# Kernel tuning notes

Measured on AMD Instinct MI355X. Metric: run time of the kernel, lower is better.

The kernel has to match this reference:

```python
import jax, jax.numpy as jnp
import numpy as np
from jax import lax

T, B, NIN, H, NOUT = 256, 64, 256, 2048, 256
DT, TAU, SIGMA = 20.0, 100.0, 0.05
DECAY = DT / TAU                      # alpha in the leaky-Euler update
NOISE_SCALE = SIGMA * float(np.sqrt(2.0 / DECAY))
MAX_INIT_STEPS = 100
ATOL = 0.1


def setup_inputs() -> dict:
    key = jax.random.key(0)
    k1, k2, k3, k4 = jax.random.split(key, 4)
    x = jax.random.normal(k1, (T, B, NIN), dtype=jnp.float32)
    W_ih = jax.random.normal(k2, (H, NIN), dtype=jnp.float32) / np.sqrt(NIN)
    # w_rec_init='diag': strong diagonal plus small random recurrent weights
    W_hh = 0.5 * jnp.eye(H, dtype=jnp.float32) + 0.1 * jax.random.normal(k3, (H, H), dtype=jnp.float32) / np.sqrt(H)
    b = jnp.zeros((H,), dtype=jnp.float32)
    W_out = jax.random.normal(k4, (NOUT, H), dtype=jnp.float32) / np.sqrt(H)
    return {"x": x, "W_ih": W_ih, "W_hh": W_hh, "b": b, "W_out": W_out}


def reference(x, W_ih, W_hh, b, W_out):
    base = jax.random.key(42)

    def cell(h, x_t, k):
        # leaky RNN step: h' = (1-a)h + a*relu(W_ih x + W_hh h + b + noise)
        pre = x_t @ W_ih.T + h @ W_hh.T + b
        pre = pre + NOISE_SCALE * jax.random.normal(k, pre.shape, dtype=pre.dtype)
        return (1.0 - DECAY) * h + DECAY * jax.nn.relu(pre)

    # ---- init_hidden_: up to 100 probe iterations of 2 steps on x[:2, 0:1] ----
    x_probe = x[:2, :1]                       # [2, 1, NIN], broadcasts vs h [B, H]
    h0_init = jnp.zeros((B, H), dtype=x.dtype)

    def init_body(carry, i):
        h0, stable, done = carry
        k = jax.random.fold_in(base, i)
        ka, kb = jax.random.split(k)
        h1 = cell(h0, x_probe[0], ka)
        h2 = cell(h1, x_probe[1], kb)
        close = jnp.max(jnp.abs(h2 - h0)) <= ATOL
        stable_new = jnp.where(done, stable, jnp.where(close, stable + 1, 0))
        trigger = (~done) & close & (stable_new >= 4)   # return pre-update h0
        done_new = done | trigger
        h0_new = jnp.where(done_new, h0, h2)
        return (h0_new, stable_new, done_new), None

    (h0, _, _), _ = lax.scan(init_body, (h0_init, jnp.int32(0), jnp.bool_(False)),
                             jnp.arange(MAX_INIT_STEPS))

    # ---- main unroll over T steps ----
    ks = jax.random.split(jax.random.fold_in(base, 1_000_000), T)

    def step(h, inp):
        x_t, k = inp
        h_new = cell(h, x_t, k)
        return h_new, h_new

    _, hidden = lax.scan(step, h0, (x, ks))   # [T, B, H]
    output = hidden @ W_out.T                 # [T, B, NOUT]
    return output, hidden
```

## Files before the change

kernel.cpp:

```cpp
#include <hip/hip_runtime.h>

typedef unsigned int u32;
typedef unsigned short u16;
typedef __bf16 bf16x8 __attribute__((ext_vector_type(8)));
typedef u16 us8 __attribute__((ext_vector_type(8)));
typedef u32 u32x4 __attribute__((ext_vector_type(4)));
typedef float f32x4 __attribute__((ext_vector_type(4)));

#define T_N 256
#define B_N 64
#define NIN_N 256
#define H_N 2048
#define NOUT_N 256
#define BH (B_N * H_N)
#define OUT_SZ (T_N * B_N * NOUT_N)

#define LDS_WHH_H 0
#define LDS_WHH_L 65536
#define LDS_RBUF  131072
#define LDS_RED   139264
#define LDS_BYTES 139328

struct U2 { u32 x, y; };

__device__ __forceinline__ u32 rotl32(u32 v, int r) { return (v << r) | (v >> (32 - r)); }

__device__ __forceinline__ U2 tf2x32(U2 k, U2 x) {
  u32 ks0 = k.x, ks1 = k.y, ks2 = k.x ^ k.y ^ 0x1BD11BDAu;
  x.x += ks0; x.y += ks1;
#define TFR(a) x.x += x.y; x.y = rotl32(x.y,(a)); x.y ^= x.x;
  TFR(13) TFR(15) TFR(26) TFR(6)
  x.x += ks1; x.y += ks2 + 1u;
  TFR(17) TFR(29) TFR(16) TFR(24)
  x.x += ks2; x.y += ks0 + 2u;
  TFR(13) TFR(15) TFR(26) TFR(6)
  x.x += ks0; x.y += ks1 + 3u;
  TFR(17) TFR(29) TFR(16) TFR(24)
  x.x += ks1; x.y += ks2 + 4u;
  TFR(13) TFR(15) TFR(26) TFR(6)
  x.x += ks2; x.y += ks0 + 5u;
#undef TFR
  return x;
}

__device__ __forceinline__ float jax_normal(u32 bits) {
  float f = __uint_as_float((bits >> 9) | 0x3f800000u) - 1.0f;
  const float lo = -0.99999994f;
  float u = fmaf(f, 2.0f, lo);
  u = fmaxf(u, lo);
  float w = -log1pf(-u * u);
  float p;
  if (w < 5.0f) {
    w = w - 2.5f;
    p =            2.81022636e-08f;
    p = fmaf(p, w, 3.43273939e-07f);
    p = fmaf(p, w, -3.5233877e-06f);
    p = fmaf(p, w, -4.39150654e-06f);
    p = fmaf(p, w, 0.00021858087f);
    p = fmaf(p, w, -0.00125372503f);
    p = fmaf(p, w, -0.00417768164f);
    p = fmaf(p, w, 0.246640727f);
    p = fmaf(p, w, 1.50140941f);
  } else {
    w = sqrtf(w) - 3.0f;
    p =            -0.000200214257f;
    p = fmaf(p, w, 0.000100950558f);
    p = fmaf(p, w, 0.00134934322f);
    p = fmaf(p, w, -0.00367342844f);
    p = fmaf(p, w, 0.00573950773f);
    p = fmaf(p, w, -0.0076224613f);
    p = fmaf(p, w, 0.00943887047f);
    p = fmaf(p, w, 1.00167406f);
    p = fmaf(p, w, 2.83297682f);
  }
  return 1.41421354f * (p * u);
}

__device__ __forceinline__ u16 f2bf(float f) {
  u32 x = __float_as_uint(f);
  u32 r = (x + 0x7FFFu + ((x >> 16) & 1u)) >> 16;
  return (u16)r;
}
__device__ __forceinline__ float bf2f(u16 b) { return __uint_as_float(((u32)b) << 16); }

__device__ __forceinline__ bf16x8 ld8(const u16* p) {
  us8 v = *reinterpret_cast<const us8*>(p);
  return __builtin_bit_cast(bf16x8, v);
}
__device__ __forceinline__ f32x4 mfma16(bf16x8 a, bf16x8 b, f32x4 c) {
  return __builtin_amdgcn_mfma_f32_16x16x32_bf16(a, b, c, 0, 0, 0);
}

__device__ __forceinline__ void st_agent_u16(u16* p, u16 v) {
  __hip_atomic_store(p, v, __ATOMIC_RELAXED, __HIP_MEMORY_SCOPE_AGENT);
}
__device__ __forceinline__ void st_agent_u32(u32* p, u32 v, int order) {
  if (order) __hip_atomic_store(p, v, __ATOMIC_RELEASE, __HIP_MEMORY_SCOPE_AGENT);
  else       __hip_atomic_store(p, v, __ATOMIC_RELAXED, __HIP_MEMORY_SCOPE_AGENT);
}
__device__ __forceinline__ u32 ld_agent_u32(const u32* p) {
  return __hip_atomic_load(p, __ATOMIC_RELAXED, __HIP_MEMORY_SCOPE_AGENT);
}

#define GLD16(AP, V) \
  asm volatile( \
    "global_load_dwordx4 %0, %16, off offset:-4096 sc0 sc1\n\t" \
    "global_load_dwordx4 %1, %16, off sc0 sc1\n\t" \
    "global_load_dwordx4 %2, %17, off offset:-4096 sc0 sc1\n\t" \
    "global_load_dwordx4 %3, %17, off sc0 sc1\n\t" \
    "global_load_dwordx4 %4, %18, off offset:-4096 sc0 sc1\n\t" \
    "global_load_dwordx4 %5, %18, off sc0 sc1\n\t" \
    "global_load_dwordx4 %6, %19, off offset:-4096 sc0 sc1\n\t" \
    "global_load_dwordx4 %7, %19, off sc0 sc1\n\t" \
    "global_load_dwordx4 %8, %20, off offset:-4096 sc0 sc1\n\t" \
    "global_load_dwordx4 %9, %20, off sc0 sc1\n\t" \
    "global_load_dwordx4 %10, %21, off offset:-4096 sc0 sc1\n\t" \
    "global_load_dwordx4 %11, %21, off sc0 sc1\n\t" \
    "global_load_dwordx4 %12, %22, off offset:-4096 sc0 sc1\n\t" \
    "global_load_dwordx4 %13, %22, off sc0 sc1\n\t" \
    "global_load_dwordx4 %14, %23, off offset:-4096 sc0 sc1\n\t" \
    "global_load_dwordx4 %15, %23, off sc0 sc1\n\t" \
    "s_waitcnt vmcnt(0)" \
    : "=&v"(V##0), "=&v"(V##1), "=&v"(V##2), "=&v"(V##3), \
      "=&v"(V##4), "=&v"(V##5), "=&v"(V##6), "=&v"(V##7), \
      "=&v"(V##8), "=&v"(V##9), "=&v"(V##10), "=&v"(V##11), \
      "=&v"(V##12), "=&v"(V##13), "=&v"(V##14), "=&v"(V##15) \
    : "v"(AP + 2048), "v"(AP + 3 * 2048), "v"(AP + 5 * 2048), "v"(AP + 7 * 2048), \
      "v"(AP + 9 * 2048), "v"(AP + 11 * 2048), "v"(AP + 13 * 2048), "v"(AP + 15 * 2048) \
    : "memory")

__global__ void __launch_bounds__(256) pack_b_kernel(const float* __restrict__ W,
    u16* __restrict__ hi, u16* __restrict__ lo, int K, int Cshift) {
  int tid = blockIdx.x * 256 + threadIdx.x;
  int lane = tid & 63;
  size_t tile = tid >> 6;
  int C = 1 << Cshift;
  int jt = (int)(tile >> Cshift), c = (int)(tile & (C - 1));
  int row = jt * 16 + (lane & 15);
  int k0 = c * 32 + (lane >> 4) * 8;
  const float* src = W + (size_t)row * K + k0;
  us8 vh, vl;
#pragma unroll
  for (int j = 0; j < 8; ++j) {
    float w = src[j];
    u16 hb = f2bf(w);
    vh[j] = hb;
    vl[j] = f2bf(w - bf2f(hb));
  }
  *reinterpret_cast<us8*>(hi + tile * 512 + lane * 8) = vh;
  *reinterpret_cast<us8*>(lo + tile * 512 + lane * 8) = vl;
}

__global__ void __launch_bounds__(256) pack_x_kernel(const float* __restrict__ x,
    u16* __restrict__ hi, u16* __restrict__ lo) {
  int tid = blockIdx.x * 256 + threadIdx.x;
  int t = tid >> 11;
  int r = tid & 2047;
  int lane = r & 63, piece = r >> 6;
  int c = piece >> 2, g = piece & 3;
  int row = g * 16 + (lane & 15);
  int k0 = c * 32 + (lane >> 4) * 8;
  const float* src = x + (size_t)t * (B_N * NIN_N) + (size_t)row * NIN_N + k0;
  us8 vh, vl;
#pragma unroll
  for (int j = 0; j < 8; ++j) {
    float w = src[j];
    u16 hb = f2bf(w);
    vh[j] = hb;
    vl[j] = f2bf(w - bf2f(hb));
  }
  size_t off = (size_t)t * 16384 + (size_t)piece * 512 + lane * 8;
  *reinterpret_cast<us8*>(hi + off) = vh;
  *reinterpret_cast<us8*>(lo + off) = vl;
}

__global__ void __launch_bounds__(256) probe_proj(const float* __restrict__ x,
    const float* __restrict__ Wih, const float* __restrict__ bias, float* __restrict__ xpj) {
  int g = blockIdx.x * 256 + threadIdx.x;
  int p = g >> 11, col = g & 2047;
  const float* xr = x + (size_t)p * (B_N * NIN_N);
  const float* wr = Wih + (size_t)col * NIN_N;
  float s = 0.f;
#pragma unroll 4
  for (int k = 0; k < NIN_N; ++k) s = fmaf(xr[k], wr[k], s);
  xpj[p * H_N + col] = s + bias[col];
}

__global__ void __launch_bounds__(256) xproj_gemm(const u16* __restrict__ xp_hi,
    const u16* __restrict__ xp_lo, const u16* __restrict__ wih_hi,
    const u16* __restrict__ wih_lo, const float* __restrict__ bias,
    float* __restrict__ xout) {
  int lane = threadIdx.x & 63, wvq = threadIdx.x >> 6;
  int t = blockIdx.x >> 7, jt16 = blockIdx.x & 127;
  const u16* ah = xp_hi + (size_t)t * 16384 + wvq * 512 + lane * 8;
  const u16* al = xp_lo + (size_t)t * 16384 + wvq * 512 + lane * 8;
  const u16* bh = wih_hi + (size_t)jt16 * 4096 + lane * 8;
  const u16* bl = wih_lo + (size_t)jt16 * 4096 + lane * 8;
  f32x4 z = {0.f, 0.f, 0.f, 0.f};
  f32x4 a0 = z, a1 = z, a2 = z;
#pragma unroll
  for (int c = 0; c < 8; ++c) {
    bf16x8 xh = ld8(ah + c * 2048), xl = ld8(al + c * 2048);
    bf16x8 wh = ld8(bh + c * 512),  wl = ld8(bl + c * 512);
    a0 = mfma16(xh, wh, a0);
    a1 = mfma16(xh, wl, a1);
    a2 = mfma16(xl, wh, a2);
  }
  f32x4 acc = (a0 + a1) + a2;
  int col = jt16 * 16 + (lane & 15);
  int q = lane >> 4;
  float bc = bias[col];
#pragma unroll
  for (int r = 0; r < 4; ++r) {
    int row = wvq * 16 + q * 4 + r;
    xout[(size_t)t * BH + (size_t)row * H_N + col] = acc[r] + bc;
  }
}

__global__ void setup_keys(U2* ka, U2* kb, U2* ks) {
  int i = threadIdx.x;
  U2 base{0u, 42u};
  if (i < 104) {
    U2 ki = tf2x32(base, U2{0u, (u32)i});
    ka[i] = tf2x32(ki, U2{0u, 0u});
    kb[i] = tf2x32(ki, U2{0u, 1u});
  }
  U2 km = tf2x32(base, U2{0u, 1000000u});
  ks[i] = tf2x32(km, U2{0u, (u32)i});
}

__global__ void __launch_bounds__(256) zero_bufs(u32* hx0w, u32* hx0lw, u32* bar) {
  int g = blockIdx.x * 256 + threadIdx.x;
  if (g < BH / 2) { hx0w[g] = 0u; hx0lw[g] = 0u; }
  if (g < 1024) bar[g] = 0u;
}

struct RnnParams {
  const u16 *whh_hi, *whh_lo;
  const float* xpj;
  float* hidden;
  u16 *hx0, *hx1, *hx2;
  u16 *hx0l, *hx1l, *hx2l;
  u16 *hxS0, *hxS1, *hxS2;
  const U2 *ka, *kb, *ks;
  u32 *slots, *mslot;
  u32 *initflag, *scanflag;
};

__global__ void __launch_bounds__(512) rnn_persistent(RnnParams P) {
  extern __shared__ char smem[];
  u16* lwhh_h = (u16*)(smem + LDS_WHH_H);
  u16* lwhh_l = (u16*)(smem + LDS_WHH_L);
  f32x4* rbuf = (f32x4*)(smem + LDS_RBUF);
  float* red  = (float*)(smem + LDS_RED);

  const int lane = threadIdx.x & 63;
  const int wv = threadIdx.x >> 6;
  const int rg = wv >> 2;
  const int kh = wv & 3;
  const int blk = blockIdx.x;
  const int jt16 = blk & 127;
  const int rh = blk >> 7;
  const int bqg = rh * 2 + rg;
  const int q = lane >> 4;
  const int row = bqg * 16 + q * 4 + kh;
  const int col = jt16 * 16 + (lane & 15);
  const u32 idx = (u32)row * H_N + (u32)col;
  const u32 xoff = ((u32)((col >> 5) * 4 + (row >> 4)) * 64
                    + (u32)(((col >> 3) & 3) * 16 + (row & 15))) * 8 + (u32)(col & 7);

  {
    const us8* sh = (const us8*)(P.whh_hi + (size_t)jt16 * 32768);
    const us8* sl = (const us8*)(P.whh_lo + (size_t)jt16 * 32768);
    us8* dh = (us8*)lwhh_h;
    us8* dl = (us8*)lwhh_l;
#pragma unroll 2
    for (int i = threadIdx.x; i < 4096; i += 512) { dh[i] = sh[i]; dl[i] = sl[i]; }
    __syncthreads();
  }
  const u16* bhp = lwhh_h + kh * 8192 + lane * 8;
  const u16* blp = lwhh_l + kh * 8192 + lane * 8;

  const u32* fl_init = P.initflag + rh * 128 + kh * 32;
  const u32* fl_scan = P.scanflag + rh * 128 + kh * 32;

  auto poll32 = [&](const u32* fl, u32 need) {
    const u32* p = fl + (lane & 31);
    for (;;) {
      u32 v;
      asm volatile("global_load_dword %0, %1, off sc0 sc1\n\ts_waitcnt vmcnt(0)"
                   : "=v"(v) : "v"(p) : "memory");
      if (__all(v >= need)) break;
      __builtin_amdgcn_s_sleep(1);
    }
  };

  auto publish = [&](u32* flagarr, u32 val) {
    asm volatile("s_waitcnt vmcnt(0)" ::: "memory");
    __syncthreads();
    if (threadIdx.x == 0) st_agent_u32(flagarr + blk, val, 1);
  };

  u32 ebar = 0;
  auto bar_agg = [&]() {
    ++ebar;
    asm volatile("s_waitcnt vmcnt(0)" ::: "memory");
    __syncthreads();
    if (wv == 0) {
      if (lane == 0) {
        float m = red[0];
#pragma unroll
        for (int w2 = 1; w2 < 8; ++w2) m = fmaxf(m, red[w2]);
        st_agent_u32(P.mslot + blk, __float_as_uint(m), 0);
        st_agent_u32(P.slots + blk, ebar, 1);
      }
      const u32* ps = P.slots + lane * 4;
      for (;;) {
        u32x4 pr;
        asm volatile("global_load_dwordx4 %0, %1, off sc0 sc1\n\ts_waitcnt vmcnt(0)"
                     : "=&v"(pr) : "v"(ps) : "memory");
        u32 mn = pr.x < pr.y ? pr.x : pr.y;
        u32 mn2 = pr.z < pr.w ? pr.z : pr.w;
        mn = mn < mn2 ? mn : mn2;
        if (__all(mn >= ebar)) break;
        __builtin_amdgcn_s_sleep(1);
      }
      float m = fmaxf(fmaxf(__uint_as_float(ld_agent_u32(P.mslot + lane * 4 + 0)),
                            __uint_as_float(ld_agent_u32(P.mslot + lane * 4 + 1))),
                      fmaxf(__uint_as_float(ld_agent_u32(P.mslot + lane * 4 + 2)),
                            __uint_as_float(ld_agent_u32(P.mslot + lane * 4 + 3))));
#pragma unroll
      for (int o = 32; o >= 1; o >>= 1) m = fmaxf(m, __shfl_down(m, o));
      if (lane == 0) ((u32*)red)[8] = (m <= 0.1f) ? 1u : 0u;
    }
    __syncthreads();
  };

  auto reduce_av = [&](f32x4 acc) -> float {
    rbuf[wv * 64 + lane] = acc;
    __syncthreads();
    const float* rb = (const float*)(rbuf + rg * 256);
    return rb[lane * 4 + kh] + rb[256 + lane * 4 + kh]
         + rb[512 + lane * 4 + kh] + rb[768 + lane * 4 + kh];
  };

  auto gemm_hi = [&](const u16* hx_in) -> float {
    const u16* ap = hx_in + bqg * 512 + kh * 32768 + lane * 8;
    u32x4 A0, A1, A2, A3, A4, A5, A6, A7, A8, A9, A10, A11, A12, A13, A14, A15;
    GLD16(ap, A);
    f32x4 z = {0.f, 0.f, 0.f, 0.f};
    f32x4 a0 = z, a1 = z, a2 = z, a3 = z;
#define HSTEP(c, AV) { bf16x8 bh_ = ld8(bhp + (c) * 512); bf16x8 bl_ = ld8(blp + (c) * 512); \
    bf16x8 ah_ = __builtin_bit_cast(bf16x8, AV); \
    if ((c) & 1) { a2 = mfma16(ah_, bh_, a2); a3 = mfma16(ah_, bl_, a3); } \
    else { a0 = mfma16(ah_, bh_, a0); a1 = mfma16(ah_, bl_, a1); } }
    HSTEP(0, A0)  HSTEP(1, A1)  HSTEP(2, A2)  HSTEP(3, A3)
    HSTEP(4, A4)  HSTEP(5, A5)  HSTEP(6, A6)  HSTEP(7, A7)
    HSTEP(8, A8)  HSTEP(9, A9)  HSTEP(10, A10) HSTEP(11, A11)
    HSTEP(12, A12) HSTEP(13, A13) HSTEP(14, A14) HSTEP(15, A15)
#undef HSTEP
    return reduce_av((a0 + a1) + (a2 + a3));
  };

  auto gemm_hilo = [&](const u16* hx_in, const u16* hx_lo) -> float {
    const u16* aph = hx_in + bqg * 512 + kh * 32768 + lane * 8;
    const u16* apl = hx_lo + bqg * 512 + kh * 32768 + lane * 8;
    f32x4 z = {0.f, 0.f, 0.f, 0.f};
    f32x4 a0 = z, a1 = z, a2 = z, a3 = z, a4 = z, a5 = z;
    {
      u32x4 H0, H1, H2, H3, H4, H5, H6, H7, H8, H9, H10, H11, H12, H13, H14, H15;
      GLD16(aph, H);
#define ISTEP(c, AV) { bf16x8 bh_ = ld8(bhp + (c) * 512); bf16x8 bl_ = ld8(blp + (c) * 512); \
      bf16x8 ah_ = __builtin_bit_cast(bf16x8, AV); \
      if ((c) & 1) { a3 = mfma16(ah_, bh_, a3); a4 = mfma16(ah_, bl_, a4); } \
      else { a0 = mfma16(ah_, bh_, a0); a1 = mfma16(ah_, bl_, a1); } }
      ISTEP(0, H0)  ISTEP(1, H1)  ISTEP(2, H2)  ISTEP(3, H3)
      ISTEP(4, H4)  ISTEP(5, H5)  ISTEP(6, H6)  ISTEP(7, H7)
      ISTEP(8, H8)  ISTEP(9, H9)  ISTEP(10, H10) ISTEP(11, H11)
      ISTEP(12, H12) ISTEP(13, H13) ISTEP(14, H14) ISTEP(15, H15)
#undef ISTEP
    }
    {
      u32x4 L0, L1, L2, L3, L4, L5, L6, L7, L8, L9, L10, L11, L12, L13, L14, L15;
      GLD16(apl, L);
#define LSTEP(c, AV) { bf16x8 bh_ = ld8(bhp + (c) * 512); \
      bf16x8 al_ = __builtin_bit_cast(bf16x8, AV); \
      if ((c) & 1) { a5 = mfma16(al_, bh_, a5); } \
      else { a2 = mfma16(al_, bh_, a2); } }
      LSTEP(0, L0)  LSTEP(1, L1)  LSTEP(2, L2)  LSTEP(3, L3)
      LSTEP(4, L4)  LSTEP(5, L5)  LSTEP(6, L6)  LSTEP(7, L7)
      LSTEP(8, L8)  LSTEP(9, L9)  LSTEP(10, L10) LSTEP(11, L11)
      LSTEP(12, L12) LSTEP(13, L13) LSTEP(14, L14) LSTEP(15, L15)
#undef LSTEP
    }
    return reduce_av(((a0 + a1) + (a2 + a3)) + (a4 + a5));
  };

  auto make_noise = [&](U2 key) -> float {
    U2 o = tf2x32(key, U2{0u, idx});
    return jax_normal(o.x ^ o.y);
  };

  const float NS = 0.15811388300841897f;
  const float xv0 = P.xpj[col];
  const float xv1 = P.xpj[H_N + col];

  u16* hxs[3]  = {P.hx0, P.hx1, P.hx2};
  u16* hxls[3] = {P.hx0l, P.hx1l, P.hx2l};
  int i0 = 0, i1 = 1, i2 = 2;
  float hp0 = 0.f;
  int stable = 0;
  float nzA = make_noise(P.ka[0]);
  float nzB = 0.f;

#pragma unroll 1
  for (int it = 0; it < 100; ++it) {
    float av = gemm_hilo(hxs[i0], hxls[i0]);
    float pre = av + xv0 + NS * nzA;
    float hp1 = 0.8f * hp0 + 0.2f * fmaxf(pre, 0.f);
    { u16 hb = f2bf(hp1);
      st_agent_u16(hxs[i1] + xoff, hb);
      st_agent_u16(hxls[i1] + xoff, f2bf(hp1 - bf2f(hb))); }
    publish(P.initflag, (u32)(it + 1));
    nzB = make_noise(P.kb[it]);
    poll32(fl_init, (u32)(it + 1));

    av = gemm_hilo(hxs[i1], hxls[i1]);
    pre = av + xv1 + NS * nzB;
    float hp2 = 0.8f * hp1 + 0.2f * fmaxf(pre, 0.f);
    { u16 hb = f2bf(hp2);
      st_agent_u16(hxs[i2] + xoff, hb);
      st_agent_u16(hxls[i2] + xoff, f2bf(hp2 - bf2f(hb))); }
    float lmax = fabsf(hp2 - hp0);
#pragma unroll
    for (int off = 32; off >= 1; off >>= 1)
      lmax = fmaxf(lmax, __shfl_down(lmax, off));
    if (lane == 0) red[wv] = lmax;
    nzA = make_noise(P.ka[it + 1]);
    bar_agg();

    bool close = (((u32*)red)[8] & 1u) != 0u;
    if (close) {
      if (++stable >= 4) break;
    } else stable = 0;
    int tmp = i0; i0 = i2; i2 = tmp;
    hp0 = hp2;
  }

  u16* bufs[3] = {P.hxS0, P.hxS1, P.hxS2};
  st_agent_u16(bufs[0] + xoff, f2bf(hp0));
  publish(P.scanflag, 1u);
  float nzS = make_noise(P.ks[0]);
  float xv = P.hidden[idx];
  float hp = hp0;
#pragma unroll 1
  for (int t = 0; t < T_N; ++t) {
    poll32(fl_scan, (u32)(t + 1));
    float av = gemm_hi(bufs[t % 3]);
    float pre = av + xv + NS * nzS;
    float hn = 0.8f * hp + 0.2f * fmaxf(pre, 0.f);
    hp = hn;
    P.hidden[(size_t)t * BH + idx] = hn;
    if (t != T_N - 1) {
      st_agent_u16(bufs[(t + 1) % 3] + xoff, f2bf(hn));
      publish(P.scanflag, (u32)(t + 2));
      nzS = make_noise(P.ks[t + 1]);
      xv = P.hidden[(size_t)(t + 1) * BH + idx];
    }
  }
}

__global__ void __launch_bounds__(256) out_gemm(const float* __restrict__ hidden,
    const u16* __restrict__ wo_hi, const u16* __restrict__ wo_lo, float* __restrict__ out) {
  int lane = threadIdx.x & 63, wv = threadIdx.x >> 6;
  int mb = blockIdx.x * 64 + wv * 16;
  int arow = mb + (lane & 15);
  int q = lane >> 4;
  f32x4 acc[16];
#pragma unroll
  for (int n = 0; n < 16; ++n) acc[n] = {0.f, 0.f, 0.f, 0.f};
  const float* ap = hidden + (size_t)arow * H_N + q * 8;
#pragma unroll 2
  for (int c = 0; c < 64; ++c) {
    const float4* a4 = reinterpret_cast<const float4*>(ap + c * 32);
    float4 f0 = a4[0], f1 = a4[1];
    us8 av;
    av[0] = f2bf(f0.x); av[1] = f2bf(f0.y); av[2] = f2bf(f0.z); av[3] = f2bf(f0.w);
    av[4] = f2bf(f1.x); av[5] = f2bf(f1.y); av[6] = f2bf(f1.z); av[7] = f2bf(f1.w);
    bf16x8 a = __builtin_bit_cast(bf16x8, av);
#pragma unroll
    for (int n = 0; n < 16; ++n) {
      bf16x8 bh = ld8(wo_hi + ((size_t)(n * 64 + c) * 64 + lane) * 8);
      bf16x8 bl = ld8(wo_lo + ((size_t)(n * 64 + c) * 64 + lane) * 8);
      acc[n] = mfma16(a, bh, acc[n]);
      acc[n] = mfma16(a, bl, acc[n]);
    }
  }
#pragma unroll
  for (int n = 0; n < 16; ++n)
#pragma unroll
    for (int r = 0; r < 4; ++r)
      out[(size_t)(mb + q * 4 + r) * NOUT_N + n * 16 + (lane & 15)] = acc[n][r];
}

extern "C" void kernel_launch(void* const* d_in, const int* in_sizes, int n_in,
                              void* d_out, int out_size, void* d_ws, size_t ws_size,
                              hipStream_t stream) {
  const float* x = (const float*)d_in[0];
  const float* W_ih = (const float*)d_in[1];
  const float* W_hh = (const float*)d_in[2];
  const float* bias = (const float*)d_in[3];
  const float* W_out = (const float*)d_in[4];
  float* out = (float*)d_out;

  char* ws = (char*)d_ws;
  size_t off = 0;
  auto alloc = [&](size_t bytes) -> void* {
    void* p = ws + off;
    off += (bytes + 255) & ~(size_t)255;
    return p;
  };
  u16* whh_hi = (u16*)alloc(8388608);
  u16* whh_lo = (u16*)alloc(8388608);
  u16* wih_hi = (u16*)alloc(1048576);
  u16* wih_lo = (u16*)alloc(1048576);
  u16* wout_hi = (u16*)alloc(1048576);
  u16* wout_lo = (u16*)alloc(1048576);
  u16* xp_hi = (u16*)alloc(8388608);
  u16* xp_lo = (u16*)alloc(8388608);
  float* xpj = (float*)alloc(16384);
  u16* hx0 = (u16*)alloc(262144);
  u16* hx1 = (u16*)alloc(262144);
  u16* hx2 = (u16*)alloc(262144);
  u16* hx0l = (u16*)alloc(262144);
  u16* hx1l = (u16*)alloc(262144);
  u16* hx2l = (u16*)alloc(262144);
  u16* hxS0 = (u16*)alloc(262144);
  u16* hxS1 = (u16*)alloc(262144);
  u16* hxS2 = (u16*)alloc(262144);
  U2* ka = (U2*)alloc(832);
  U2* kb = (U2*)alloc(832);
  U2* ks = (U2*)alloc(2048);
  u32* bar = (u32*)alloc(4096);

  float* hidden = out + OUT_SZ;

  hipLaunchKernelGGL(pack_b_kernel, dim3(2048), dim3(256), 0, stream, W_hh, whh_hi, whh_lo, 2048, 6);
  hipLaunchKernelGGL(pack_b_kernel, dim3(256), dim3(256), 0, stream, W_ih, wih_hi, wih_lo, 256, 3);
  hipLaunchKernelGGL(pack_b_kernel, dim3(256), dim3(256), 0, stream, W_out, wout_hi, wout_lo, 2048, 6);
  hipLaunchKernelGGL(pack_x_kernel, dim3(2048), dim3(256), 0, stream, x, xp_hi, xp_lo);
  hipLaunchKernelGGL(probe_proj, dim3(16), dim3(256), 0, stream, x, W_ih, bias, xpj);
  hipLaunchKernelGGL(setup_keys, dim3(1), dim3(256), 0, stream, ka, kb, ks);
  hipLaunchKernelGGL(zero_bufs, dim3(256), dim3(256), 0, stream, (u32*)hx0, (u32*)hx0l, bar);
  hipLaunchKernelGGL(xproj_gemm, dim3(32768), dim3(256), 0, stream, xp_hi, xp_lo, wih_hi, wih_lo, bias, hidden);

  RnnParams P;
  P.whh_hi = whh_hi; P.whh_lo = whh_lo;
  P.xpj = xpj;
  P.hidden = hidden;
  P.hx0 = hx0; P.hx1 = hx1; P.hx2 = hx2;
  P.hx0l = hx0l; P.hx1l = hx1l; P.hx2l = hx2l;
  P.hxS0 = hxS0; P.hxS1 = hxS1; P.hxS2 = hxS2;
  P.ka = ka; P.kb = kb; P.ks = ks;
  P.slots = bar; P.mslot = bar + 256;
  P.initflag = bar + 512; P.scanflag = bar + 768;

  static bool attr_set = false;
  if (!attr_set) {
    hipFuncSetAttribute((const void*)rnn_persistent,
                        hipFuncAttributeMaxDynamicSharedMemorySize, LDS_BYTES);
    attr_set = true;
  }

  void* kargs[] = {(void*)&P};
  hipLaunchCooperativeKernel((const void*)rnn_persistent, dim3(256), dim3(512), kargs, LDS_BYTES, stream);

  hipLaunchKernelGGL(out_gemm, dim3(256), dim3(256), 0, stream, hidden, wout_hi, wout_lo, out);
}
```

Baseline: 4.955 ms.

## Repartition persistent RNN blocks by batch group with full-K split and narrower flag polling

Each block now owns a 16-row batch group and 32 hidden columns, with its eight waves splitting the full K dimension. Previously blocks split batch into halves and covered 16 columns with a four-way K split. The W_hh hi part is kept in LDS while the lo correction is read from global memory. Each block now waits on only 8 producer flags per wave instead of 32, cutting dependency fan-in and poll traffic, and the hidden-state store is moved after publishing the next step's flag. The cost is an 8-way LDS reduction and global loads of the lo weights on every step, which may add latency.

```diff
diff --git a/kernel.cpp b/kernel.cpp
--- a/kernel.cpp
+++ b/kernel.cpp
@@ -15,11 +15,10 @@
 #define BH (B_N * H_N)
 #define OUT_SZ (T_N * B_N * NOUT_N)
 
-#define LDS_WHH_H 0
-#define LDS_WHH_L 65536
-#define LDS_RBUF  131072
-#define LDS_RED   139264
-#define LDS_BYTES 139328
+#define LDS_W    0
+#define LDS_RBUF 131072
+#define LDS_RED  147456
+#define LDS_BYTES 147520
 
 struct U2 { u32 x, y; };
 
@@ -102,7 +101,23 @@
   return __hip_atomic_load(p, __ATOMIC_RELAXED, __HIP_MEMORY_SCOPE_AGENT);
 }
 
-#define GLD16(AP, V) \
+#define GLD8(AP, V) \
+  asm volatile( \
+    "global_load_dwordx4 %0, %8, off offset:-4096 sc0 sc1\n\t" \
+    "global_load_dwordx4 %1, %8, off sc0 sc1\n\t" \
+    "global_load_dwordx4 %2, %9, off offset:-4096 sc0 sc1\n\t" \
+    "global_load_dwordx4 %3, %9, off sc0 sc1\n\t" \
+    "global_load_dwordx4 %4, %10, off offset:-4096 sc0 sc1\n\t" \
+    "global_load_dwordx4 %5, %10, off sc0 sc1\n\t" \
+    "global_load_dwordx4 %6, %11, off offset:-4096 sc0 sc1\n\t" \
+    "global_load_dwordx4 %7, %11, off sc0 sc1\n\t" \
+    "s_waitcnt vmcnt(0)" \
+    : "=&v"(V##0), "=&v"(V##1), "=&v"(V##2), "=&v"(V##3), \
+      "=&v"(V##4), "=&v"(V##5), "=&v"(V##6), "=&v"(V##7) \
+    : "v"(AP + 2048), "v"(AP + 3 * 2048), "v"(AP + 5 * 2048), "v"(AP + 7 * 2048) \
+    : "memory")
+
+#define GLD8HL(APH, APL, V, W) \
   asm volatile( \
     "global_load_dwordx4 %0, %16, off offset:-4096 sc0 sc1\n\t" \
     "global_load_dwordx4 %1, %16, off sc0 sc1\n\t" \
@@ -123,10 +138,10 @@
     "s_waitcnt vmcnt(0)" \
     : "=&v"(V##0), "=&v"(V##1), "=&v"(V##2), "=&v"(V##3), \
       "=&v"(V##4), "=&v"(V##5), "=&v"(V##6), "=&v"(V##7), \
-      "=&v"(V##8), "=&v"(V##9), "=&v"(V##10), "=&v"(V##11), \
-      "=&v"(V##12), "=&v"(V##13), "=&v"(V##14), "=&v"(V##15) \
-    : "v"(AP + 2048), "v"(AP + 3 * 2048), "v"(AP + 5 * 2048), "v"(AP + 7 * 2048), \
-      "v"(AP + 9 * 2048), "v"(AP + 11 * 2048), "v"(AP + 13 * 2048), "v"(AP + 15 * 2048) \
+      "=&v"(W##0), "=&v"(W##1), "=&v"(W##2), "=&v"(W##3), \
+      "=&v"(W##4), "=&v"(W##5), "=&v"(W##6), "=&v"(W##7) \
+    : "v"(APH + 2048), "v"(APH + 3 * 2048), "v"(APH + 5 * 2048), "v"(APH + 7 * 2048), \
+      "v"(APL + 2048), "v"(APL + 3 * 2048), "v"(APL + 5 * 2048), "v"(APL + 7 * 2048) \
     : "memory")
 
 __global__ void __launch_bounds__(256) pack_b_kernel(const float* __restrict__ W,
@@ -249,43 +264,45 @@
 
 __global__ void __launch_bounds__(512) rnn_persistent(RnnParams P) {
   extern __shared__ char smem[];
-  u16* lwhh_h = (u16*)(smem + LDS_WHH_H);
-  u16* lwhh_l = (u16*)(smem + LDS_WHH_L);
+  u16* lW = (u16*)(smem + LDS_W);
   f32x4* rbuf = (f32x4*)(smem + LDS_RBUF);
   float* red  = (float*)(smem + LDS_RED);
 
-  const int lane = threadIdx.x & 63;
-  const int wv = threadIdx.x >> 6;
-  const int rg = wv >> 2;
-  const int kh = wv & 3;
+  const int tid = threadIdx.x;
+  const int lane = tid & 63;
+  const int wv = tid >> 6;
+  const int ke = wv;
+  const int cs_own = wv >> 2;
+  const int r_own = wv & 3;
   const int blk = blockIdx.x;
-  const int jt16 = blk & 127;
-  const int rh = blk >> 7;
-  const int bqg = rh * 2 + rg;
-  const int q = lane >> 4;
-  const int row = bqg * 16 + q * 4 + kh;
-  const int col = jt16 * 16 + (lane & 15);
+  const int bg = blk >> 6;
+  const int ct = blk & 63;
+  const int row = bg * 16 + (lane >> 4) * 4 + r_own;
+  const int col = ct * 32 + cs_own * 16 + (lane & 15);
   const u32 idx = (u32)row * H_N + (u32)col;
   const u32 xoff = ((u32)((col >> 5) * 4 + (row >> 4)) * 64
                     + (u32)(((col >> 3) & 3) * 16 + (row & 15))) * 8 + (u32)(col & 7);
 
   {
-    const us8* sh = (const us8*)(P.whh_hi + (size_t)jt16 * 32768);
-    const us8* sl = (const us8*)(P.whh_lo + (size_t)jt16 * 32768);
-    us8* dh = (us8*)lwhh_h;
-    us8* dl = (us8*)lwhh_l;
-#pragma unroll 2
-    for (int i = threadIdx.x; i < 4096; i += 512) { dh[i] = sh[i]; dl[i] = sl[i]; }
+    const us8* src = (const us8*)P.whh_hi;
+    us8* dst = (us8*)lW;
+#pragma unroll 4
+    for (int i = tid; i < 8192; i += 512) {
+      int cs_ = i >> 12, rem = i & 4095;
+      dst[i] = src[(size_t)(ct * 2 + cs_) * 4096 + rem];
+    }
     __syncthreads();
   }
-  const u16* bhp = lwhh_h + kh * 8192 + lane * 8;
-  const u16* blp = lwhh_l + kh * 8192 + lane * 8;
-
-  const u32* fl_init = P.initflag + rh * 128 + kh * 32;
-  const u32* fl_scan = P.scanflag + rh * 128 + kh * 32;
-
-  auto poll32 = [&](const u32* fl, u32 need) {
-    const u32* p = fl + (lane & 31);
+  const u16* lwb0 = lW + ke * 4096 + lane * 8;
+  const u16* lwb1 = lW + 32768 + ke * 4096 + lane * 8;
+  const u16* wlo0 = P.whh_lo + (size_t)(ct * 2 + 0) * 32768 + ke * 4096 + lane * 8;
+  const u16* wlo1 = P.whh_lo + (size_t)(ct * 2 + 1) * 32768 + ke * 4096 + lane * 8;
+
+  const u32* ifw = P.initflag + bg * 64 + ke * 8;
+  const u32* sfw = P.scanflag + bg * 64 + ke * 8;
+
+  auto pollW = [&](const u32* fw, u32 need) {
+    const u32* p = fw + (lane & 7);
     for (;;) {
       u32 v;
       asm volatile("global_load_dword %0, %1, off sc0 sc1\n\ts_waitcnt vmcnt(0)"
@@ -298,7 +315,7 @@
   auto publish = [&](u32* flagarr, u32 val) {
     asm volatile("s_waitcnt vmcnt(0)" ::: "memory");
     __syncthreads();
-    if (threadIdx.x == 0) st_agent_u32(flagarr + blk, val, 1);
+    if (tid == 0) st_agent_u32(flagarr + blk, val, 1);
   };
 
   u32 ebar = 0;
@@ -336,64 +353,75 @@
     __syncthreads();
   };
 
-  auto reduce_av = [&](f32x4 acc) -> float {
-    rbuf[wv * 64 + lane] = acc;
+  auto reduce_sum = [&](f32x4 o0, f32x4 o1) -> float {
+    rbuf[(wv * 2 + 0) * 64 + lane] = o0;
+    rbuf[(wv * 2 + 1) * 64 + lane] = o1;
     __syncthreads();
-    const float* rb = (const float*)(rbuf + rg * 256);
-    return rb[lane * 4 + kh] + rb[256 + lane * 4 + kh]
-         + rb[512 + lane * 4 + kh] + rb[768 + lane * 4 + kh];
-  };
-
-  auto gemm_hi = [&](const u16* hx_in) -> float {
-    const u16* ap = hx_in + bqg * 512 + kh * 32768 + lane * 8;
-    u32x4 A0, A1, A2, A3, A4, A5, A6, A7, A8, A9, A10, A11, A12, A13, A14, A15;
-    GLD16(ap, A);
+    const float* rb = (const float*)rbuf;
+    int o = cs_own * 256 + lane * 4 + r_own;
+    float av = rb[o];
+    av += rb[o + 512];  av += rb[o + 1024]; av += rb[o + 1536];
+    av += rb[o + 2048]; av += rb[o + 2560]; av += rb[o + 3072]; av += rb[o + 3584];
+    return av;
+  };
+
+  auto gemm_sc = [&](const u16* hx_in, f32x4& o0, f32x4& o1) {
+    const u16* ap = hx_in + bg * 512 + ke * 16384 + lane * 8;
+    u32x4 A0, A1, A2, A3, A4, A5, A6, A7;
+    GLD8(ap, A);
     f32x4 z = {0.f, 0.f, 0.f, 0.f};
-    f32x4 a0 = z, a1 = z, a2 = z, a3 = z;
-#define HSTEP(c, AV) { bf16x8 bh_ = ld8(bhp + (c) * 512); bf16x8 bl_ = ld8(blp + (c) * 512); \
-    bf16x8 ah_ = __builtin_bit_cast(bf16x8, AV); \
-    if ((c) & 1) { a2 = mfma16(ah_, bh_, a2); a3 = mfma16(ah_, bl_, a3); } \
-    else { a0 = mfma16(ah_, bh_, a0); a1 = mfma16(ah_, bl_, a1); } }
-    HSTEP(0, A0)  HSTEP(1, A1)  HSTEP(2, A2)  HSTEP(3, A3)
-    HSTEP(4, A4)  HSTEP(5, A5)  HSTEP(6, A6)  HSTEP(7, A7)
-    HSTEP(8, A8)  HSTEP(9, A9)  HSTEP(10, A10) HSTEP(11, A11)
-    HSTEP(12, A12) HSTEP(13, A13) HSTEP(14, A14) HSTEP(15, A15)
-#undef HSTEP
-    return reduce_av((a0 + a1) + (a2 + a3));
-  };
-
-  auto gemm_hilo = [&](const u16* hx_in, const u16* hx_lo) -> float {
-    const u16* aph = hx_in + bqg * 512 + kh * 32768 + lane * 8;
-    const u16* apl = hx_lo + bqg * 512 + kh * 32768 + lane * 8;
+    {
+      f32x4 a0 = z, a1 = z, a2 = z, a3 = z;
+#define SSTEP(j, AV) { bf16x8 bh_ = ld8(lwb0 + (j) * 512); bf16x8 bl_ = ld8(wlo0 + (j) * 512); \
+      bf16x8 ah_ = __builtin_bit_cast(bf16x8, AV); \
+      if ((j) & 1) { a2 = mfma16(ah_, bh_, a2); a3 = mfma16(ah_, bl_, a3); } \
+      else { a0 = mfma16(ah_, bh_, a0); a1 = mfma16(ah_, bl_, a1); } }
+      SSTEP(0, A0) SSTEP(1, A1) SSTEP(2, A2) SSTEP(3, A3)
+      SSTEP(4, A4) SSTEP(5, A5) SSTEP(6, A6) SSTEP(7, A7)
+#undef SSTEP
+      o0 = (a0 + a1) + (a2 + a3);
+    }
+    {
+      f32x4 a0 = z, a1 = z, a2 = z, a3 = z;
+#define SSTEP(j, AV) { bf16x8 bh_ = ld8(lwb1 + (j) * 512); bf16x8 bl_ = ld8(wlo1 + (j) * 512); \
+      bf16x8 ah_ = __builtin_bit_cast(bf16x8, AV); \
+      if ((j) & 1) { a2 = mfma16(ah_, bh_, a2); a3 = mfma16(ah_, bl_, a3); } \
+      else { a0 = mfma16(ah_, bh_, a0); a1 = mfma16(ah_, bl_, a1); } }
+      SSTEP(0, A0) SSTEP(1, A1) SSTEP(2, A2) SSTEP(3, A3)
+      SSTEP(4, A4) SSTEP(5, A5) SSTEP(6, A6) SSTEP(7, A7)
+#undef SSTEP
+      o1 = (a0 + a1) + (a2 + a3);
+    }
+  };
+
+  auto gemm_in = [&](const u16* hxh, const u16* hxl, f32x4& o0, f32x4& o1) {
+    const u16* aph = hxh + bg * 512 + ke * 16384 + lane * 8;
+    const u16* apl = hxl + bg * 512 + ke * 16384 + lane * 8;
+    u32x4 H0, H1, H2, H3, H4, H5, H6, H7, L0, L1, L2, L3, L4, L5, L6, L7;
+    GLD8HL(aph, apl, H, L);
     f32x4 z = {0.f, 0.f, 0.f, 0.f};
-    f32x4 a0 = z, a1 = z, a2 = z, a3 = z, a4 = z, a5 = z;
     {
-      u32x4 H0, H1, H2, H3, H4, H5, H6, H7, H8, H9, H10, H11, H12, H13, H14, H15;
-      GLD16(aph, H);
-#define ISTEP(c, AV) { bf16x8 bh_ = ld8(bhp + (c) * 512); bf16x8 bl_ = ld8(blp + (c) * 512); \
-      bf16x8 ah_ = __builtin_bit_cast(bf16x8, AV); \
-      if ((c) & 1) { a3 = mfma16(ah_, bh_, a3); a4 = mfma16(ah_, bl_, a4); } \
-      else { a0 = mfma16(ah_, bh_, a0); a1 = mfma16(ah_, bl_, a1); } }
-      ISTEP(0, H0)  ISTEP(1, H1)  ISTEP(2, H2)  ISTEP(3, H3)
-      ISTEP(4, H4)  ISTEP(5, H5)  ISTEP(6, H6)  ISTEP(7, H7)
-      ISTEP(8, H8)  ISTEP(9, H9)  ISTEP(10, H10) ISTEP(11, H11)
-      ISTEP(12, H12) ISTEP(13, H13) ISTEP(14, H14) ISTEP(15, H15)
+      f32x4 a0 = z, a1 = z, a2 = z, a3 = z, a4 = z, a5 = z;
+#define ISTEP(j, AV, LV) { bf16x8 bh_ = ld8(lwb0 + (j) * 512); bf16x8 bl_ = ld8(wlo0 + (j) * 512); \
+      bf16x8 ah_ = __builtin_bit_cast(bf16x8, AV); bf16x8 al_ = __builtin_bit_cast(bf16x8, LV); \
+      if ((j) & 1) { a3 = mfma16(ah_, bh_, a3); a4 = mfma16(ah_, bl_, a4); a5 = mfma16(al_, bh_, a5); } \
+      else { a0 = mfma16(ah_, bh_, a0); a1 = mfma16(ah_, bl_, a1); a2 = mfma16(al_, bh_, a2); } }
+      ISTEP(0, H0, L0) ISTEP(1, H1, L1) ISTEP(2, H2, L2) ISTEP(3, H3, L3)
+      ISTEP(4, H4, L4) ISTEP(5, H5, L5) ISTEP(6, H6, L6) ISTEP(7, H7, L7)
 #undef ISTEP
+      o0 = ((a0 + a1) + (a2 + a3)) + (a4 + a5);
     }
     {
-      u32x4 L0, L1, L2, L3, L4, L5, L6, L7, L8, L9, L10, L11, L12, L13, L14, L15;
-      GLD16(apl, L);
-#define LSTEP(c, AV) { bf16x8 bh_ = ld8(bhp + (c) * 512); \
-      bf16x8 al_ = __builtin_bit_cast(bf16x8, AV); \
-      if ((c) & 1) { a5 = mfma16(al_, bh_, a5); } \
-      else { a2 = mfma16(al_, bh_, a2); } }
-      LSTEP(0, L0)  LSTEP(1, L1)  LSTEP(2, L2)  LSTEP(3, L3)
-      LSTEP(4, L4)  LSTEP(5, L5)  LSTEP(6, L6)  LSTEP(7, L7)
-      LSTEP(8, L8)  LSTEP(9, L9)  LSTEP(10, L10) LSTEP(11, L11)
-      LSTEP(12, L12) LSTEP(13, L13) LSTEP(14, L14) LSTEP(15, L15)
-#undef LSTEP
-    }
-    return reduce_av(((a0 + a1) + (a2 + a3)) + (a4 + a5));
+      f32x4 a0 = z, a1 = z, a2 = z, a3 = z, a4 = z, a5 = z;
+#define ISTEP(j, AV, LV) { bf16x8 bh_ = ld8(lwb1 + (j) * 512); bf16x8 bl_ = ld8(wlo1 + (j) * 512); \
+      bf16x8 ah_ = __builtin_bit_cast(bf16x8, AV); bf16x8 al_ = __builtin_bit_cast(bf16x8, LV); \
+      if ((j) & 1) { a3 = mfma16(ah_, bh_, a3); a4 = mfma16(ah_, bl_, a4); a5 = mfma16(al_, bh_, a5); } \
+      else { a0 = mfma16(ah_, bh_, a0); a1 = mfma16(ah_, bl_, a1); a2 = mfma16(al_, bh_, a2); } }
+      ISTEP(0, H0, L0) ISTEP(1, H1, L1) ISTEP(2, H2, L2) ISTEP(3, H3, L3)
+      ISTEP(4, H4, L4) ISTEP(5, H5, L5) ISTEP(6, H6, L6) ISTEP(7, H7, L7)
+#undef ISTEP
+      o1 = ((a0 + a1) + (a2 + a3)) + (a4 + a5);
+    }
   };
 
   auto make_noise = [&](U2 key) -> float {
@@ -415,7 +443,9 @@
 
 #pragma unroll 1
   for (int it = 0; it < 100; ++it) {
-    float av = gemm_hilo(hxs[i0], hxls[i0]);
+    f32x4 o0, o1;
+    gemm_in(hxs[i0], hxls[i0], o0, o1);
+    float av = reduce_sum(o0, o1);
     float pre = av + xv0 + NS * nzA;
     float hp1 = 0.8f * hp0 + 0.2f * fmaxf(pre, 0.f);
     { u16 hb = f2bf(hp1);
@@ -423,9 +453,10 @@
       st_agent_u16(hxls[i1] + xoff, f2bf(hp1 - bf2f(hb))); }
     publish(P.initflag, (u32)(it + 1));
     nzB = make_noise(P.kb[it]);
-    poll32(fl_init, (u32)(it + 1));
-
-    av = gemm_hilo(hxs[i1], hxls[i1]);
+    pollW(ifw, (u32)(it + 1));
+
+    gemm_in(hxs[i1], hxls[i1], o0, o1);
+    av = reduce_sum(o0, o1);
     pre = av + xv1 + NS * nzB;
     float hp2 = 0.8f * hp1 + 0.2f * fmaxf(pre, 0.f);
     { u16 hb = f2bf(hp2);
@@ -455,17 +486,21 @@
   float hp = hp0;
 #pragma unroll 1
   for (int t = 0; t < T_N; ++t) {
-    poll32(fl_scan, (u32)(t + 1));
-    float av = gemm_hi(bufs[t % 3]);
+    pollW(sfw, (u32)(t + 1));
+    f32x4 o0, o1;
+    gemm_sc(bufs[t % 3], o0, o1);
+    float av = reduce_sum(o0, o1);
     float pre = av + xv + NS * nzS;
     float hn = 0.8f * hp + 0.2f * fmaxf(pre, 0.f);
     hp = hn;
-    P.hidden[(size_t)t * BH + idx] = hn;
     if (t != T_N - 1) {
       st_agent_u16(bufs[(t + 1) % 3] + xoff, f2bf(hn));
       publish(P.scanflag, (u32)(t + 2));
+      P.hidden[(size_t)t * BH + idx] = hn;
       nzS = make_noise(P.ks[t + 1]);
       xv = P.hidden[(size_t)(t + 1) * BH + idx];
+    } else {
+      P.hidden[(size_t)t * BH + idx] = hn;
     }
   }
 }
```

Result: faster. 4.812 ms (-2.9%).
